# Kernel optimization log

Measured on AMD Instinct MI355X. Metric: run time of the kernel, lower is better.

## Reference

```python
import jax, jax.numpy as jnp
import numpy as np

B, TQ, TK = 8, 256, 256
DQ, DK, DV, H = 512, 512, 512, 256


def setup_inputs() -> dict:
    key = jax.random.key(0)
    k1, k2, k3, k4, k5, k6 = jax.random.split(key, 6)
    queries = jax.random.normal(k1, (B, TQ, DQ), dtype=jnp.float32)
    keys = jax.random.normal(k2, (B, TK, DK), dtype=jnp.float32)
    values = jax.random.normal(k3, (B, TK, DV), dtype=jnp.float32)
    # Linear(in, out, bias=False): y = x @ W.T with W (out,in); store transposed (in,out)
    Wq = jax.random.normal(k4, (DQ, H), dtype=jnp.float32) / np.sqrt(DQ)
    Wk = jax.random.normal(k5, (DK, H), dtype=jnp.float32) / np.sqrt(DK)
    wv = jax.random.normal(k6, (H,), dtype=jnp.float32) / np.sqrt(H)
    return {"queries": queries, "keys": keys, "values": values,
            "Wq": Wq, "Wk": Wk, "wv": wv}


def reference(queries, keys, values, Wq, Wk, wv):
    q = jnp.einsum('bqd,dh->bqh', queries, Wq)          # (B,Tq,H)
    k = jnp.einsum('bkd,dh->bkh', keys, Wk)             # (B,Tk,H)
    features = jnp.tanh(q[:, :, None, :] + k[:, None, :, :])  # (B,Tq,Tk,H)
    scores = jnp.einsum('bqkh,h->bqk', features, wv)    # (B,Tq,Tk)
    attn = jax.nn.softmax(scores, axis=-1)              # (B,Tq,Tk)
    return jnp.einsum('bqk,bkv->bqv', attn, values)     # (B,Tq,Dv)
```

## Files before the change

kernel.cpp:

```cpp
#include <hip/hip_runtime.h>

typedef float v2f __attribute__((ext_vector_type(2)));
typedef short bf16x8 __attribute__((ext_vector_type(8)));
typedef float f32x4 __attribute__((ext_vector_type(4)));

namespace {
constexpr int B   = 8;
constexpr int TQ  = 256;
constexpr int TK  = 256;
constexpr int DQK = 512;
constexpr int DV  = 512;
constexpr int H   = 256;
constexpr int QB  = 4;
constexpr float C2LOG2E   = 2.8853900817779268f;
constexpr float NEG2LOG2E = -2.8853900817779268f;
}

__device__ __forceinline__ uint32_t f2u(float x) { return __builtin_bit_cast(uint32_t, x); }
__device__ __forceinline__ float u2f(uint32_t x) { return __builtin_bit_cast(float, x); }
__device__ __forceinline__ uint32_t pack_hi(float x, float y) {
    return (f2u(y) & 0xFFFF0000u) | (f2u(x) >> 16);
}

__global__ __launch_bounds__(256)
void proj_kernel(const float* __restrict__ Q, const float* __restrict__ Kin,
                 const float* __restrict__ Wq, const float* __restrict__ Wk,
                 float* __restrict__ qpc, float* __restrict__ kpc4)
{
    __shared__ short Ahi[4][64][8];
    __shared__ short Alo[4][64][8];
    __shared__ short Bhi[4][32][8];
    __shared__ short Blo[4][32][8];

    const bool kside = (blockIdx.z == 1);
    const float* A = kside ? Kin : Q;
    const float* W = kside ? Wk  : Wq;
    const int m0 = blockIdx.x * 64;
    const int n0 = blockIdx.y * 32;
    const int tid = threadIdx.x;

    const int am = tid >> 2, ag = tid & 3;
    const int bk = tid >> 3, bn4 = (tid & 7) * 4;
    const float4* aptr = (const float4*)(A + (m0 + am) * DQK) + ag * 2;
    const float*  wptr = W + bk * H + n0 + bn4;

    const int w = tid >> 6, l = tid & 63;
    const int wm = (w >> 1) * 32, wn = (w & 1) * 16;
    const int fg = l >> 4;
    const int fr = l & 15;

    float4 a0 = aptr[0], a1 = aptr[1];
    float4 bv = *(const float4*)wptr;

    f32x4 acc0 = {0.f, 0.f, 0.f, 0.f};
    f32x4 acc1 = {0.f, 0.f, 0.f, 0.f};

    for (int s = 0; s < 16; ++s) {
        __syncthreads();
        {
            float ah0 = u2f(f2u(a0.x) & 0xFFFF0000u), ah1 = u2f(f2u(a0.y) & 0xFFFF0000u);
            float ah2 = u2f(f2u(a0.z) & 0xFFFF0000u), ah3 = u2f(f2u(a0.w) & 0xFFFF0000u);
            float ah4 = u2f(f2u(a1.x) & 0xFFFF0000u), ah5 = u2f(f2u(a1.y) & 0xFFFF0000u);
            float ah6 = u2f(f2u(a1.z) & 0xFFFF0000u), ah7 = u2f(f2u(a1.w) & 0xFFFF0000u);
            int4 hw, lw;
            hw.x = (int)pack_hi(a0.x, a0.y); hw.y = (int)pack_hi(a0.z, a0.w);
            hw.z = (int)pack_hi(a1.x, a1.y); hw.w = (int)pack_hi(a1.z, a1.w);
            lw.x = (int)pack_hi(a0.x - ah0, a0.y - ah1);
            lw.y = (int)pack_hi(a0.z - ah2, a0.w - ah3);
            lw.z = (int)pack_hi(a1.x - ah4, a1.y - ah5);
            lw.w = (int)pack_hi(a1.z - ah6, a1.w - ah7);
            *(int4*)&Ahi[ag][am][0] = hw;
            *(int4*)&Alo[ag][am][0] = lw;
            const int g = bk >> 3, slot = bk & 7;
            float bb[4] = {bv.x, bv.y, bv.z, bv.w};
            #pragma unroll
            for (int i = 0; i < 4; ++i) {
                uint32_t u = f2u(bb[i]);
                float hf = u2f(u & 0xFFFF0000u);
                Bhi[g][bn4 + i][slot] = (short)(u >> 16);
                Blo[g][bn4 + i][slot] = (short)(f2u(bb[i] - hf) >> 16);
            }
        }
        __syncthreads();
        if (s < 15) {
            a0 = aptr[s * 8 + 8];
            a1 = aptr[s * 8 + 9];
            bv = *(const float4*)(wptr + (s + 1) * 32 * H);
        }
        bf16x8 ah_0 = *(const bf16x8*)&Ahi[fg][wm + fr][0];
        bf16x8 ah_1 = *(const bf16x8*)&Ahi[fg][wm + 16 + fr][0];
        bf16x8 al_0 = *(const bf16x8*)&Alo[fg][wm + fr][0];
        bf16x8 al_1 = *(const bf16x8*)&Alo[fg][wm + 16 + fr][0];
        bf16x8 bh   = *(const bf16x8*)&Bhi[fg][wn + fr][0];
        bf16x8 bl   = *(const bf16x8*)&Blo[fg][wn + fr][0];
        acc0 = __builtin_amdgcn_mfma_f32_16x16x32_bf16(ah_0, bh, acc0, 0, 0, 0);
        acc1 = __builtin_amdgcn_mfma_f32_16x16x32_bf16(ah_1, bh, acc1, 0, 0, 0);
        acc0 = __builtin_amdgcn_mfma_f32_16x16x32_bf16(ah_0, bl, acc0, 0, 0, 0);
        acc1 = __builtin_amdgcn_mfma_f32_16x16x32_bf16(ah_1, bl, acc1, 0, 0, 0);
        acc0 = __builtin_amdgcn_mfma_f32_16x16x32_bf16(al_0, bh, acc0, 0, 0, 0);
        acc1 = __builtin_amdgcn_mfma_f32_16x16x32_bf16(al_1, bh, acc1, 0, 0, 0);
    }

    const int col = n0 + wn + fr;
    #pragma unroll
    for (int mi = 0; mi < 2; ++mi) {
        f32x4 acc = mi ? acc1 : acc0;
        #pragma unroll
        for (int r = 0; r < 4; ++r) {
            const int row = m0 + wm + mi * 16 + fg * 4 + r;
            float val = __builtin_amdgcn_exp2f(acc[r] * C2LOG2E);
            if (!kside) {
                qpc[row * H + col] = val;
            } else {
                const int bb2 = row >> 8, kk = row & 255;
                kpc4[((bb2 * (H / 4) + (col >> 2)) * TK + kk) * 4 + (col & 3)] = val;
            }
        }
    }
}

__global__ __launch_bounds__(512)
void attn_kernel(const float* __restrict__ qpc, const float* __restrict__ kpc4,
                 const float* __restrict__ wv, const float* __restrict__ values,
                 float* __restrict__ out)
{
    __shared__ float qlds[H][QB];
    __shared__ float wlds[H];
    __shared__ float accbuf[4][QB][TK];
    __shared__ float pT[TK][QB];
    __shared__ float rowsum[QB];

    const int b   = blockIdx.x >> 6;
    const int q0  = (blockIdx.x & 63) * QB;
    const int tid = threadIdx.x;

    for (int i = tid; i < QB * H; i += 512) {
        const int h = i >> 2, q = i & 3;
        qlds[h][q] = qpc[(b * TQ + q0 + q) * H + h];
    }
    if (tid < H) wlds[tid] = wv[tid];
    if (tid < QB) rowsum[tid] = 0.0f;
    __syncthreads();

    {
        const int kp = tid & 127;
        const int hg = tid >> 7;
        const int h0 = hg * 64;
        const float4* kc = (const float4*)kpc4 + (b * (H / 4) + (h0 >> 2)) * TK + 2 * kp;
        v2f a01a = {0.f, 0.f}, a23a = {0.f, 0.f};
        v2f a01b = {0.f, 0.f}, a23b = {0.f, 0.f};
        #pragma unroll 4
        for (int h4 = 0; h4 < 16; ++h4) {
            float4 kva4 = kc[h4 * TK];
            float4 kvb4 = kc[h4 * TK + 1];
            #pragma unroll
            for (int j = 0; j < 4; ++j) {
                const int h = h0 + h4 * 4 + j;
                const float ea = (j == 0) ? kva4.x : (j == 1) ? kva4.y : (j == 2) ? kva4.z : kva4.w;
                const float eb = (j == 0) ? kvb4.x : (j == 1) ? kvb4.y : (j == 2) ? kvb4.z : kvb4.w;
                const float wj = wlds[h];
                float4 qa = *(const float4*)&qlds[h][0];
                v2f q01 = {qa.x, qa.y}, q23 = {qa.z, qa.w};
                v2f ea2 = {ea, ea}, eb2 = {eb, eb}, w2 = {wj, wj};
                v2f one = {1.0f, 1.0f};
                v2f d0a = __builtin_elementwise_fma(q01, ea2, one);
                v2f d1a = __builtin_elementwise_fma(q23, ea2, one);
                v2f d0b = __builtin_elementwise_fma(q01, eb2, one);
                v2f d1b = __builtin_elementwise_fma(q23, eb2, one);
                v2f r0a, r1a, r0b, r1b;
                r0a.x = __builtin_amdgcn_rcpf(d0a.x);
                r0a.y = __builtin_amdgcn_rcpf(d0a.y);
                r1a.x = __builtin_amdgcn_rcpf(d1a.x);
                r1a.y = __builtin_amdgcn_rcpf(d1a.y);
                r0b.x = __builtin_amdgcn_rcpf(d0b.x);
                r0b.y = __builtin_amdgcn_rcpf(d0b.y);
                r1b.x = __builtin_amdgcn_rcpf(d1b.x);
                r1b.y = __builtin_amdgcn_rcpf(d1b.y);
                a01a = __builtin_elementwise_fma(w2, r0a, a01a);
                a23a = __builtin_elementwise_fma(w2, r1a, a23a);
                a01b = __builtin_elementwise_fma(w2, r0b, a01b);
                a23b = __builtin_elementwise_fma(w2, r1b, a23b);
            }
        }
        accbuf[hg][0][2 * kp]     = a01a.x;
        accbuf[hg][1][2 * kp]     = a01a.y;
        accbuf[hg][2][2 * kp]     = a23a.x;
        accbuf[hg][3][2 * kp]     = a23a.y;
        accbuf[hg][0][2 * kp + 1] = a01b.x;
        accbuf[hg][1][2 * kp + 1] = a01b.y;
        accbuf[hg][2][2 * kp + 1] = a23b.x;
        accbuf[hg][3][2 * kp + 1] = a23b.y;
    }
    __syncthreads();

    for (int i = tid; i < QB * TK; i += 512) {
        const int kk = i >> 2, q = i & 3;
        float s = (accbuf[0][q][kk] + accbuf[1][q][kk]) +
                  (accbuf[2][q][kk] + accbuf[3][q][kk]);
        float e = __builtin_amdgcn_exp2f(s * NEG2LOG2E);
        pT[kk][q] = e;
        float r = e;
        r += __shfl_xor(r, 4);
        r += __shfl_xor(r, 8);
        r += __shfl_xor(r, 16);
        r += __shfl_xor(r, 32);
        if ((tid & 63) < 4) atomicAdd(&rowsum[tid & 63], r);
    }
    __syncthreads();

    {
        const int c = tid;
        const float* vb = values + b * TK * DV + c;
        float o0 = 0.f, o1 = 0.f, o2 = 0.f, o3 = 0.f;
        #pragma unroll 4
        for (int kk = 0; kk < TK; ++kk) {
            float v = vb[kk * DV];
            float4 p4 = *(const float4*)&pT[kk][0];
            o0 = fmaf(p4.x, v, o0);
            o1 = fmaf(p4.y, v, o1);
            o2 = fmaf(p4.z, v, o2);
            o3 = fmaf(p4.w, v, o3);
        }
        float* ob = out + (b * TQ + q0) * DV + c;
        ob[0 * DV] = o0 * __builtin_amdgcn_rcpf(rowsum[0]);
        ob[1 * DV] = o1 * __builtin_amdgcn_rcpf(rowsum[1]);
        ob[2 * DV] = o2 * __builtin_amdgcn_rcpf(rowsum[2]);
        ob[3 * DV] = o3 * __builtin_amdgcn_rcpf(rowsum[3]);
    }
}

extern "C" void kernel_launch(void* const* d_in, const int* in_sizes, int n_in,
                              void* d_out, int out_size, void* d_ws, size_t ws_size,
                              hipStream_t stream)
{
    const float* queries = (const float*)d_in[0];
    const float* keys    = (const float*)d_in[1];
    const float* values  = (const float*)d_in[2];
    const float* Wq      = (const float*)d_in[3];
    const float* Wk      = (const float*)d_in[4];
    const float* wv      = (const float*)d_in[5];
    float* out  = (float*)d_out;
    float* qpc  = (float*)d_ws;
    float* kpc4 = qpc + B * TQ * H;

    dim3 gproj(B * TQ / 64, H / 32, 2);
    proj_kernel<<<gproj, 256, 0, stream>>>(queries, keys, Wq, Wk, qpc, kpc4);
    attn_kernel<<<B * (TQ / QB), 512, 0, stream>>>(qpc, kpc4, wv, values, out);
}
```

Measured before the change: 56.83 us.

## Split attention over key halves with partial outputs and a separate epilogue

Each attention block now handles one half of the keys for a group of four queries, which doubles the grid to 1024 blocks. Each block writes unnormalized partial outputs and partial row sums to workspace, and a new epilogue kernel combines the halves and normalizes. The aim is more parallelism and occupancy (launch bounds now request 8 waves per EU) and less per-block serial work in the score loop. The cost is an extra kernel launch and about 8 MB of extra global traffic for the partial outputs. The softmax still has no max subtraction, as before.

```diff
diff --git a/kernel.cpp b/kernel.cpp
--- a/kernel.cpp
+++ b/kernel.cpp
@@ -119,19 +119,21 @@
     }
 }
 
-__global__ __launch_bounds__(512)
+__global__ __launch_bounds__(512, 8)
 void attn_kernel(const float* __restrict__ qpc, const float* __restrict__ kpc4,
                  const float* __restrict__ wv, const float* __restrict__ values,
-                 float* __restrict__ out)
+                 float* __restrict__ opart, float* __restrict__ rs_g)
 {
     __shared__ float qlds[H][QB];
     __shared__ float wlds[H];
-    __shared__ float accbuf[4][QB][TK];
-    __shared__ float pT[TK][QB];
-    __shared__ float rowsum[QB];
-
-    const int b   = blockIdx.x >> 6;
-    const int q0  = (blockIdx.x & 63) * QB;
+    __shared__ float accbuf[8][QB][128];
+    __shared__ float elds[QB][128];
+
+    const int bid = blockIdx.x;
+    const int b   = bid >> 7;
+    const int qg  = (bid >> 1) & 63;
+    const int kh  = bid & 1;
+    const int q0  = qg * QB;
     const int tid = threadIdx.x;
 
     for (int i = tid; i < QB * H; i += 512) {
@@ -139,26 +141,27 @@
         qlds[h][q] = qpc[(b * TQ + q0 + q) * H + h];
     }
     if (tid < H) wlds[tid] = wv[tid];
-    if (tid < QB) rowsum[tid] = 0.0f;
     __syncthreads();
 
     {
-        const int kp = tid & 127;
-        const int hg = tid >> 7;
-        const int h0 = hg * 64;
-        const float4* kc = (const float4*)kpc4 + (b * (H / 4) + (h0 >> 2)) * TK + 2 * kp;
+        const int kp = tid & 63;
+        const int hg = tid >> 6;
+        const int h0 = hg * 32;
+        const float4* kc = (const float4*)kpc4 + (b * (H / 4) + hg * 8) * TK
+                           + (kh * 128 + 2 * kp);
         v2f a01a = {0.f, 0.f}, a23a = {0.f, 0.f};
         v2f a01b = {0.f, 0.f}, a23b = {0.f, 0.f};
         #pragma unroll 4
-        for (int h4 = 0; h4 < 16; ++h4) {
+        for (int h4 = 0; h4 < 8; ++h4) {
             float4 kva4 = kc[h4 * TK];
             float4 kvb4 = kc[h4 * TK + 1];
+            float4 w4 = *(const float4*)&wlds[h0 + h4 * 4];
             #pragma unroll
             for (int j = 0; j < 4; ++j) {
                 const int h = h0 + h4 * 4 + j;
                 const float ea = (j == 0) ? kva4.x : (j == 1) ? kva4.y : (j == 2) ? kva4.z : kva4.w;
                 const float eb = (j == 0) ? kvb4.x : (j == 1) ? kvb4.y : (j == 2) ? kvb4.z : kvb4.w;
-                const float wj = wlds[h];
+                const float wj = (j == 0) ? w4.x  : (j == 1) ? w4.y  : (j == 2) ? w4.z  : w4.w;
                 float4 qa = *(const float4*)&qlds[h][0];
                 v2f q01 = {qa.x, qa.y}, q23 = {qa.z, qa.w};
                 v2f ea2 = {ea, ea}, eb2 = {eb, eb}, w2 = {wj, wj};
@@ -193,40 +196,64 @@
     }
     __syncthreads();
 
-    for (int i = tid; i < QB * TK; i += 512) {
-        const int kk = i >> 2, q = i & 3;
-        float s = (accbuf[0][q][kk] + accbuf[1][q][kk]) +
-                  (accbuf[2][q][kk] + accbuf[3][q][kk]);
-        float e = __builtin_amdgcn_exp2f(s * NEG2LOG2E);
-        pT[kk][q] = e;
-        float r = e;
-        r += __shfl_xor(r, 4);
-        r += __shfl_xor(r, 8);
-        r += __shfl_xor(r, 16);
-        r += __shfl_xor(r, 32);
-        if ((tid & 63) < 4) atomicAdd(&rowsum[tid & 63], r);
+    {
+        const int q = tid >> 7, kl = tid & 127;
+        float s = ((accbuf[0][q][kl] + accbuf[1][q][kl]) +
+                   (accbuf[2][q][kl] + accbuf[3][q][kl])) +
+                  ((accbuf[4][q][kl] + accbuf[5][q][kl]) +
+                   (accbuf[6][q][kl] + accbuf[7][q][kl]));
+        elds[q][kl] = __builtin_amdgcn_exp2f(s * NEG2LOG2E);
     }
     __syncthreads();
 
     {
+        const int wave = tid >> 6, lane = tid & 63;
+        if (wave < QB) {
+            float s = elds[wave][lane] + elds[wave][lane + 64];
+            #pragma unroll
+            for (int off = 1; off < 64; off <<= 1)
+                s += __shfl_xor(s, off);
+            if (lane == 0) rs_g[(b * TQ + q0 + wave) * 2 + kh] = s;
+        }
+    }
+
+    {
         const int c = tid;
-        const float* vb = values + b * TK * DV + c;
+        const float* vb = values + (b * TK + kh * 128) * DV + c;
         float o0 = 0.f, o1 = 0.f, o2 = 0.f, o3 = 0.f;
         #pragma unroll 4
-        for (int kk = 0; kk < TK; ++kk) {
+        for (int kk = 0; kk < 128; ++kk) {
             float v = vb[kk * DV];
-            float4 p4 = *(const float4*)&pT[kk][0];
-            o0 = fmaf(p4.x, v, o0);
-            o1 = fmaf(p4.y, v, o1);
-            o2 = fmaf(p4.z, v, o2);
-            o3 = fmaf(p4.w, v, o3);
-        }
-        float* ob = out + (b * TQ + q0) * DV + c;
-        ob[0 * DV] = o0 * __builtin_amdgcn_rcpf(rowsum[0]);
-        ob[1 * DV] = o1 * __builtin_amdgcn_rcpf(rowsum[1]);
-        ob[2 * DV] = o2 * __builtin_amdgcn_rcpf(rowsum[2]);
-        ob[3 * DV] = o3 * __builtin_amdgcn_rcpf(rowsum[3]);
-    }
+            o0 = fmaf(elds[0][kk], v, o0);
+            o1 = fmaf(elds[1][kk], v, o1);
+            o2 = fmaf(elds[2][kk], v, o2);
+            o3 = fmaf(elds[3][kk], v, o3);
+        }
+        float* ob = opart + kh * (B * TQ * DV) + (b * TQ + q0) * DV + c;
+        ob[0 * DV] = o0;
+        ob[1 * DV] = o1;
+        ob[2 * DV] = o2;
+        ob[3 * DV] = o3;
+    }
+}
+
+__global__ __launch_bounds__(256)
+void epilogue_kernel(const float* __restrict__ opart, const float* __restrict__ rs_g,
+                     float* __restrict__ out)
+{
+    const int idx4 = blockIdx.x * 256 + threadIdx.x;
+    const int row  = idx4 >> 7;
+    float rs = rs_g[2 * row] + rs_g[2 * row + 1];
+    float inv = __builtin_amdgcn_rcpf(rs);
+    const float4* o0 = (const float4*)opart;
+    const float4* o1 = (const float4*)(opart + B * TQ * DV);
+    float4 a = o0[idx4], bq = o1[idx4];
+    float4 r;
+    r.x = (a.x + bq.x) * inv;
+    r.y = (a.y + bq.y) * inv;
+    r.z = (a.z + bq.z) * inv;
+    r.w = (a.w + bq.w) * inv;
+    ((float4*)out)[idx4] = r;
 }
 
 extern "C" void kernel_launch(void* const* d_in, const int* in_sizes, int n_in,
@@ -239,11 +266,14 @@
     const float* Wq      = (const float*)d_in[3];
     const float* Wk      = (const float*)d_in[4];
     const float* wv      = (const float*)d_in[5];
-    float* out  = (float*)d_out;
-    float* qpc  = (float*)d_ws;
-    float* kpc4 = qpc + B * TQ * H;
+    float* out   = (float*)d_out;
+    float* qpc   = (float*)d_ws;
+    float* kpc4  = qpc + B * TQ * H;
+    float* opart = kpc4 + B * H * TK;
+    float* rs_g  = opart + 2 * B * TQ * DV;
 
     dim3 gproj(B * TQ / 64, H / 32, 2);
     proj_kernel<<<gproj, 256, 0, stream>>>(queries, keys, Wq, Wk, qpc, kpc4);
-    attn_kernel<<<B * (TQ / QB), 512, 0, stream>>>(qpc, kpc4, wv, values, out);
-}
+    attn_kernel<<<B * (TQ / QB) * 2, 512, 0, stream>>>(qpc, kpc4, wv, values, opart, rs_g);
+    epilogue_kernel<<<B * TQ * DV / 4 / 256, 256, 0, stream>>>(opart, rs_g, out);
+}
```

Measured after the change: 54.92 us. 3.4% less time.
